# Kernel optimization log

Measured on AMD Instinct MI355X. Metric: run time of the kernel, lower is better.

The kernel has to match this reference:

```python
import jax, jax.numpy as jnp
import numpy as np

N = 50000       # nodes
E = 500000      # edges (before self-loops)
F_IN = 128      # node feature dim
F_E = 16        # edge feature dim
H = 8           # heads (conv1, conv2)
C1 = 32         # 256 // 8
C2 = 16         # 128 // 8
OUT = 1         # conv3 output channels (1 head, concat=False)
NS = 0.2        # leaky_relu negative slope
EPS = 1e-5      # batchnorm eps


def setup_inputs() -> dict:
    key = jax.random.key(0)
    ks = jax.random.split(key, 32)
    r = lambda k, s: jax.random.normal(k, s, jnp.float32) * 0.1
    inp = {
        'x': jax.random.normal(ks[0], (N, F_IN), jnp.float32),
        'edge_index': jax.random.randint(ks[1], (2, E), 0, N, jnp.int32),
        'edge_attr': jax.random.normal(ks[2], (E, F_E), jnp.float32),
        # conv1 (share_weights=True -> single lin)
        'W1': r(ks[3], (F_IN, H * C1)), 'b1': jnp.zeros((H * C1,), jnp.float32),
        'We1': r(ks[4], (F_E, H * C1)), 'att1': r(ks[5], (H, C1)),
        'bo1': jnp.zeros((H * C1,), jnp.float32),
        'g1': jnp.ones((H * C1,), jnp.float32), 'bt1': jnp.zeros((H * C1,), jnp.float32),
        # conv2 (share_weights=True)
        'W2': r(ks[6], (H * C1, H * C2)), 'b2': jnp.zeros((H * C2,), jnp.float32),
        'We2': r(ks[7], (F_E, H * C2)), 'att2': r(ks[8], (H, C2)),
        'bo2': jnp.zeros((H * C2,), jnp.float32),
        'g2': jnp.ones((H * C2,), jnp.float32), 'bt2': jnp.zeros((H * C2,), jnp.float32),
        # conv3 (share_weights=False -> separate lin_l / lin_r; 1 head, concat=False)
        'W3l': r(ks[9], (H * C2, OUT)), 'b3l': jnp.zeros((OUT,), jnp.float32),
        'W3r': r(ks[10], (H * C2, OUT)), 'b3r': jnp.zeros((OUT,), jnp.float32),
        'We3': r(ks[11], (F_E, OUT)), 'att3': r(ks[12], (1, OUT)),
        'bo3': jnp.zeros((OUT,), jnp.float32),
    }
    return inp


def _gatv2(x, src, dst, eattr, Wl, bl, Wr, br, We, att, bo, heads, ch, concat):
    """One GATv2Conv layer (PyG semantics), edges already include self-loops."""
    n = x.shape[0]
    xl = (x @ Wl + bl).reshape(n, heads, ch)              # source transform
    xr = (x @ Wr + br).reshape(n, heads, ch)              # target transform
    e = (eattr @ We).reshape(-1, heads, ch)               # edge transform (no bias)
    m = xl[src] + xr[dst] + e                             # [Etot, H, C]
    logit = jnp.einsum('ehc,hc->eh', jax.nn.leaky_relu(m, NS), att)
    lmax = jax.ops.segment_max(logit, dst, num_segments=n)
    ex = jnp.exp(logit - lmax[dst])
    denom = jax.ops.segment_sum(ex, dst, num_segments=n)
    alpha = ex / (denom[dst] + 1e-16)                     # segment softmax over dst
    out = jax.ops.segment_sum(alpha[:, :, None] * xl[src], dst, num_segments=n)
    out = out.reshape(n, heads * ch) if concat else out.mean(axis=1)
    return out + bo


def _bn(x, g, b):
    mu = x.mean(axis=0)
    var = ((x - mu) ** 2).mean(axis=0)
    return g * (x - mu) * jax.lax.rsqrt(var + EPS) + b


def reference(x, edge_index, edge_attr, W1, b1, We1, att1, bo1, g1, bt1,
              W2, b2, We2, att2, bo2, g2, bt2,
              W3l, b3l, W3r, b3r, We3, att3, bo3):
    n = x.shape[0]
    # add_self_loops=True with fill_value='mean' for edge_attr (PyG default)
    loop = jnp.arange(n, dtype=edge_index.dtype)
    src = jnp.concatenate([edge_index[0], loop])
    dst = jnp.concatenate([edge_index[1], loop])
    ea = jnp.concatenate([edge_attr,
                          jnp.broadcast_to(edge_attr.mean(axis=0), (n, edge_attr.shape[1]))], axis=0)

    h = _gatv2(x, src, dst, ea, W1, b1, W1, b1, We1, att1, bo1, H, C1, True)
    h = jax.nn.elu(_bn(h, g1, bt1))
    h = _gatv2(h, src, dst, ea, W2, b2, W2, b2, We2, att2, bo2, H, C2, True)
    h = jax.nn.elu(_bn(h, g2, bt2))
    out = _gatv2(h, src, dst, ea, W3l, b3l, W3r, b3r, We3, att3, bo3, 1, OUT, False)
    return out  # [N, 1]
```

## Files before the change

kernel.cpp:

```cpp
#include <hip/hip_runtime.h>

typedef unsigned short u16;
typedef __attribute__((ext_vector_type(4))) float f32x4;
typedef __attribute__((ext_vector_type(2))) float f32x2;
typedef __attribute__((ext_vector_type(8))) short bf16x8;

constexpr int Nn  = 50000;
constexpr int Ee  = 500000;
constexpr int ET  = Nn + Ee;
constexpr int FIN = 128;
constexpr int FE  = 16;
constexpr int Hh  = 8;
constexpr int C1  = 32, HC1 = 256;
constexpr int C2  = 16, HC2 = 128;
constexpr float NS  = 0.2f;
constexpr float EPS = 1e-5f;

__device__ __forceinline__ float b2f(u16 u) { return __uint_as_float(((unsigned)u) << 16); }
__device__ __forceinline__ u16 f2b(float f) {
  unsigned u = __float_as_uint(f);
  u += 0x7FFF + ((u >> 16) & 1);
  return (u16)(u >> 16);
}
__device__ __forceinline__ f32x2 ldbf2(const u16* p) {
  ushort2 u = *reinterpret_cast<const ushort2*>(p);
  return (f32x2){b2f(u.x), b2f(u.y)};
}
__device__ __forceinline__ void stbf2(u16* p, f32x2 v) {
  ushort2 u; u.x = f2b(v.x); u.y = f2b(v.y);
  *reinterpret_cast<ushort2*>(p) = u;
}

template <int RED>
__device__ __forceinline__ float red_sum(float v) {
  v += __int_as_float(__builtin_amdgcn_update_dpp(0, __float_as_int(v), 0xB1, 0xF, 0xF, true));
  v += __int_as_float(__builtin_amdgcn_update_dpp(0, __float_as_int(v), 0x4E, 0xF, 0xF, true));
  v += __int_as_float(__builtin_amdgcn_update_dpp(0, __float_as_int(v), 0x141, 0xF, 0xF, true));
  if constexpr (RED == 16)
    v += __int_as_float(__builtin_amdgcn_update_dpp(0, __float_as_int(v), 0x140, 0xF, 0xF, true));
  return v;
}

__global__ void k_init(int* __restrict__ deg, int* __restrict__ cursor, float* __restrict__ ea_mean,
                       float* __restrict__ bn1s, float* __restrict__ bn1q,
                       float* __restrict__ bn2s, float* __restrict__ bn2q) {
  int t = blockIdx.x * 256 + threadIdx.x;
  int stride = gridDim.x * 256;
  for (int i = t; i < Nn; i += stride) { deg[i] = 0; cursor[i] = 0; }
  if (t < FE) ea_mean[t] = 0.f;
  if (t >= 64 && t < 64 + HC1) { bn1s[t - 64] = 0.f; bn1q[t - 64] = 0.f; }
  if (t >= 384 && t < 384 + HC2) { bn2s[t - 384] = 0.f; bn2q[t - 384] = 0.f; }
}

__global__ void k_deg_mean(const int* __restrict__ ei, const float* __restrict__ ea,
                           int* __restrict__ deg, float* __restrict__ ea_mean) {
  int t = threadIdx.x;
  int e = blockIdx.x * 256 + t;
  if (e < ET) {
    int d = (e < Ee) ? ei[Ee + e] : (e - Ee);
    if ((unsigned)d >= (unsigned)Nn) d = 0;
    atomicAdd(&deg[d], 1);
  }
  __shared__ float s[256];
  int f  = t & 15;
  int r0 = (t >> 4) + blockIdx.x * 16;
  float acc = 0.f;
  for (int r = r0; r < Ee; r += gridDim.x * 16) acc += ea[r * FE + f];
  s[t] = acc;
  __syncthreads();
  if (t < 16) {
    float v = 0.f;
    for (int r = 0; r < 16; r++) v += s[r * 16 + t];
    atomicAdd(&ea_mean[t], v * (1.f / Ee));
  }
}

__global__ __launch_bounds__(1024) void k_scan(const int* __restrict__ deg, int* __restrict__ rowptr) {
  const int T = 1024;
  int t = threadIdx.x;
  const int CH = (Nn + T - 1) / T;
  int base = t * CH;
  int sum = 0;
  for (int i = 0; i < CH; i++) {
    int idx = base + i;
    if (idx < Nn) sum += deg[idx];
  }
  __shared__ int s[T];
  s[t] = sum;
  __syncthreads();
  for (int off = 1; off < T; off <<= 1) {
    int v = (t >= off) ? s[t - off] : 0;
    __syncthreads();
    s[t] += v;
    __syncthreads();
  }
  int run = (t == 0) ? 0 : s[t - 1];
  for (int i = 0; i < CH; i++) {
    int idx = base + i;
    if (idx < Nn) { rowptr[idx] = run; run += deg[idx]; }
  }
  if (t == T - 1) rowptr[Nn] = run;
}

__global__ void k_scatter(const int* __restrict__ ei, const int* __restrict__ rowptr,
                          int* __restrict__ cursor, int2* __restrict__ epack) {
  int e = blockIdx.x * 256 + threadIdx.x;
  if (e >= ET) return;
  int s, d;
  if (e < Ee) { s = ei[e]; d = ei[Ee + e]; } else { s = d = e - Ee; }
  if ((unsigned)s >= (unsigned)Nn) s = 0;
  if ((unsigned)d >= (unsigned)Nn) d = 0;
  int pos = rowptr[d] + atomicAdd(&cursor[d], 1);
  epack[pos] = make_int2(s, e);
}

__global__ void k_bn_coef(const float* __restrict__ sum, const float* __restrict__ sq,
                          const float* __restrict__ g, const float* __restrict__ bt,
                          float2* __restrict__ coef, int HC) {
  int ch = threadIdx.x;
  if (ch >= HC) return;
  float mu = sum[ch] * (1.f / Nn);
  float var = sq[ch] * (1.f / Nn) - mu * mu;
  float rs = rsqrtf(var + EPS);
  float sc = g[ch] * rs;
  coef[ch] = make_float2(sc, bt[ch] - sc * mu);
}

template <int HC>
__global__ void k_bn_stats(const u16* __restrict__ x, float* __restrict__ sum, float* __restrict__ sq) {
  long e0 = (long)blockIdx.x * 256 + threadIdx.x;
  long stride = (long)gridDim.x * 256;
  float s = 0.f, s2 = 0.f;
  for (long e = e0; e < (long)Nn * HC; e += stride) {
    float v = b2f(x[e]);
    s += v; s2 += v * v;
  }
  int ch = (int)(e0 % HC);
  atomicAdd(&sum[ch], s);
  atomicAdd(&sq[ch], s2);
}

template <int KK, int NN, typename AT, bool FUSE>
__global__ __launch_bounds__(256) void k_gemm_mfma(const AT* __restrict__ A, const float* __restrict__ W,
                                                   const float* __restrict__ bias, u16* __restrict__ C,
                                                   const float2* __restrict__ coef, int M) {
  constexpr int WT = KK + 8;
  __shared__ u16 Wt[64 * WT];
  int tid = threadIdx.x;
  int col0 = blockIdx.x * 64;
  int row0 = blockIdx.y * 64;
  for (int idx = tid; idx < KK * 64; idx += 256) {
    int k = idx >> 6, c = idx & 63;
    Wt[c * WT + k] = f2b(W[(size_t)k * NN + col0 + c]);
  }
  __syncthreads();
  int lane = tid & 63;
  int w = tid >> 6;
  int mr = lane & 15, quad = lane >> 4;
  int row = row0 + w * 16 + mr;
  f32x4 acc[4];
#pragma unroll
  for (int t = 0; t < 4; t++) acc[t] = (f32x4){0.f, 0.f, 0.f, 0.f};
  union Frag { bf16x8 v; u16 u[8]; };
  for (int kb = 0; kb < KK; kb += 32) {
    Frag a;
    if (row < M) {
      if constexpr (sizeof(AT) == 4) {
        const float* ap = (const float*)&A[(size_t)row * KK + kb + quad * 8];
        float4 a0 = *reinterpret_cast<const float4*>(ap);
        float4 a1 = *reinterpret_cast<const float4*>(ap + 4);
        a.u[0] = f2b(a0.x); a.u[1] = f2b(a0.y); a.u[2] = f2b(a0.z); a.u[3] = f2b(a0.w);
        a.u[4] = f2b(a1.x); a.u[5] = f2b(a1.y); a.u[6] = f2b(a1.z); a.u[7] = f2b(a1.w);
      } else {
        a.v = *reinterpret_cast<const bf16x8*>(&A[(size_t)row * KK + kb + quad * 8]);
        if constexpr (FUSE) {
          int k0 = kb + quad * 8;
#pragma unroll
          for (int j = 0; j < 8; j++) {
            float2 c2 = coef[k0 + j];
            float y = b2f(a.u[j]) * c2.x + c2.y;
            y = y > 0.f ? y : __expf(y) - 1.f;
            a.u[j] = f2b(y);
          }
        }
      }
    } else {
#pragma unroll
      for (int j = 0; j < 8; j++) a.u[j] = 0;
    }
#pragma unroll
    for (int t = 0; t < 4; t++) {
      const bf16x8* bp = reinterpret_cast<const bf16x8*>(&Wt[(t * 16 + mr) * WT + kb + quad * 8]);
      acc[t] = __builtin_amdgcn_mfma_f32_16x16x32_bf16(a.v, *bp, acc[t], 0, 0, 0);
    }
  }
  int orow = row0 + w * 16 + quad * 4;
#pragma unroll
  for (int t = 0; t < 4; t++) {
    int col = col0 + t * 16 + mr;
    float bs = bias[col];
#pragma unroll
    for (int r = 0; r < 4; r++) {
      int rr = orow + r;
      if (rr < M) C[(size_t)rr * NN + col] = f2b(acc[t][r] + bs);
    }
  }
}

template <int HC, int C, int WPN>
__global__ __launch_bounds__(256) void k_node_attn(
    const int* __restrict__ rowptr, const int2* __restrict__ epack,
    const u16* __restrict__ xl, const float* __restrict__ We, const float* __restrict__ att,
    const float* __restrict__ edge_attr, const float* __restrict__ ea_mean,
    const float* __restrict__ bo, u16* __restrict__ out) {
  int lane = threadIdx.x & 63;
  int gwid = (blockIdx.x << 2) + (threadIdx.x >> 6);
  int nwaves = gridDim.x << 2;
  int w = gwid % WPN;
  int i0 = gwid / WPN;
  int istride = nwaves / WPN;
  int c0 = w * 128 + lane * 2;
  f32x2 w2[FE];
#pragma unroll
  for (int k = 0; k < FE; k++) {
    float2 t = *reinterpret_cast<const float2*>(&We[k * HC + c0]);
    w2[k] = (f32x2){t.x, t.y};
  }
  float at0 = att[c0], at1 = att[c0 + 1];
  f32x2 ews2 = {0.f, 0.f};
#pragma unroll
  for (int k = 0; k < FE; k++) ews2 += ea_mean[k] * w2[k];
  float b0 = bo[c0], b1 = bo[c0 + 1];
  constexpr int RED = C / 2;
  constexpr int UN = 4;

  auto edge_ew = [&](int eid) -> f32x2 {
    if (eid < Ee) {
      const float4* ep = reinterpret_cast<const float4*>(&edge_attr[(size_t)eid * FE]);
      f32x2 a = {0.f, 0.f};
#pragma unroll
      for (int k4 = 0; k4 < 4; k4++) {
        float4 u = ep[k4];
        a += u.x * w2[4 * k4 + 0];
        a += u.y * w2[4 * k4 + 1];
        a += u.z * w2[4 * k4 + 2];
        a += u.w * w2[4 * k4 + 3];
      }
      return a;
    }
    return ews2;
  };

  if (i0 >= Nn) return;
  int p0 = rowptr[i0], p1 = rowptr[i0 + 1];
  ushort2 xdr = *reinterpret_cast<const ushort2*>(&xl[(size_t)i0 * HC + c0]);

  for (int i = i0; i < Nn;) {
    int inext = i + istride;
    int np0 = 0, np1 = 0;
    ushort2 nxdr = make_ushort2(0, 0);
    if (inext < Nn) {
      np0 = rowptr[inext];
      np1 = rowptr[inext + 1];
      nxdr = *reinterpret_cast<const ushort2*>(&xl[(size_t)inext * HC + c0]);
    }
    f32x2 xd = (f32x2){b2f(xdr.x), b2f(xdr.y)};
    int nb = (p1 - p0 + UN - 1) >> 2;
    float m = -1e30f, l = 0.f;
    f32x2 acc = {0.f, 0.f};

    int2 se[UN];
    int pb = p0;
#pragma unroll
    for (int j = 0; j < UN; j++) se[j] = epack[min(pb + j, p1 - 1)];

    for (int b = 0; b < nb; b++) {
      int sA[UN], eA[UN];
#pragma unroll
      for (int j = 0; j < UN; j++) {
        sA[j] = __builtin_amdgcn_readfirstlane(se[j].x);
        eA[j] = __builtin_amdgcn_readfirstlane(se[j].y);
      }
      ushort2 xr[UN];
#pragma unroll
      for (int j = 0; j < UN; j++)
        xr[j] = *reinterpret_cast<const ushort2*>(&xl[(size_t)sA[j] * HC + c0]);
      int pn = pb + UN;
      if (pn < p1) {
#pragma unroll
        for (int j = 0; j < UN; j++) se[j] = epack[min(pn + j, p1 - 1)];
      }
      f32x2 ew[UN];
#pragma unroll
      for (int j = 0; j < UN; j++) ew[j] = edge_ew(eA[j]);
      f32x2 xs[UN];
      float part[UN];
#pragma unroll
      for (int j = 0; j < UN; j++) {
        xs[j] = (f32x2){b2f(xr[j].x), b2f(xr[j].y)};
        f32x2 t = xs[j] + xd + ew[j];
        f32x2 tn = t * NS;
        f32x2 lk = {fmaxf(t.x, tn.x), fmaxf(t.y, tn.y)};
        float pt = lk.x * at0 + lk.y * at1;
        pt = red_sum<RED>(pt);
        part[j] = (pb + j < p1) ? pt : -1e30f;
      }
      float mn = m;
#pragma unroll
      for (int j = 0; j < UN; j++) mn = fmaxf(mn, part[j]);
      float sc = __expf(m - mn);
      float a[UN], asum = 0.f;
      f32x2 ax = {0.f, 0.f};
#pragma unroll
      for (int j = 0; j < UN; j++) {
        a[j] = __expf(part[j] - mn);
        asum += a[j];
        ax += a[j] * xs[j];
      }
      l = l * sc + asum;
      acc = acc * sc + ax;
      m = mn;
      pb = pn;
    }
    float inv = 1.f / (l + 1e-16f);
    f32x2 v = {acc.x * inv + b0, acc.y * inv + b1};
    stbf2(&out[(size_t)i * HC + c0], v);
    i = inext; p0 = np0; p1 = np1; xdr = nxdr;
  }
}

__global__ __launch_bounds__(256) void k_gemv3(const u16* __restrict__ h2,
                                               const float2* __restrict__ coef,
                                               const float* __restrict__ W3l, const float* __restrict__ b3l,
                                               const float* __restrict__ W3r, const float* __restrict__ b3r,
                                               float* __restrict__ xl3, float* __restrict__ xr3) {
  int lane = threadIdx.x & 63;
  int i = (blockIdx.x << 2) + (threadIdx.x >> 6);
  if (i >= Nn) return;
  float2 ca = coef[lane], cb = coef[64 + lane];
  float a = b2f(h2[(long)i * HC2 + lane]) * ca.x + ca.y;
  a = a > 0.f ? a : __expf(a) - 1.f;
  float b = b2f(h2[(long)i * HC2 + 64 + lane]) * cb.x + cb.y;
  b = b > 0.f ? b : __expf(b) - 1.f;
  float pl = a * W3l[lane] + b * W3l[64 + lane];
  float pr = a * W3r[lane] + b * W3r[64 + lane];
  for (int o = 1; o < 64; o <<= 1) { pl += __shfl_xor(pl, o); pr += __shfl_xor(pr, o); }
  if (lane == 0) { xl3[i] = pl + b3l[0]; xr3[i] = pr + b3r[0]; }
}

__global__ __launch_bounds__(256) void k_final3(
    const int* __restrict__ rowptr, const int2* __restrict__ epack,
    const float* __restrict__ xl3, const float* __restrict__ xr3,
    const float* __restrict__ We3, const float* __restrict__ att3,
    const float* __restrict__ edge_attr, const float* __restrict__ ea_mean,
    const float* __restrict__ bo3, float* __restrict__ out) {
  int lane = threadIdx.x & 63;
  int i = (blockIdx.x << 2) + (threadIdx.x >> 6);
  if (i >= Nn) return;
  float we[FE];
#pragma unroll
  for (int k4 = 0; k4 < 4; k4++) {
    float4 u = reinterpret_cast<const float4*>(We3)[k4];
    we[4 * k4] = u.x; we[4 * k4 + 1] = u.y; we[4 * k4 + 2] = u.z; we[4 * k4 + 3] = u.w;
  }
  float at = att3[0];
  float ews = 0.f;
#pragma unroll
  for (int k = 0; k < FE; k++) ews += ea_mean[k] * we[k];
  float xd = xr3[i];
  int p0 = rowptr[i], p1 = rowptr[i + 1];
  float m = -1e30f, l = 0.f, o = 0.f;
  for (int p = p0 + lane; p < p1; p += 64) {
    int2 se = epack[p];
    int s = se.x, eid = se.y;
    float ew;
    if (eid < Ee) {
      const float4* ep = reinterpret_cast<const float4*>(&edge_attr[(size_t)eid * FE]);
      ew = 0.f;
#pragma unroll
      for (int k4 = 0; k4 < 4; k4++) {
        float4 u = ep[k4];
        ew += u.x * we[4 * k4] + u.y * we[4 * k4 + 1] + u.z * we[4 * k4 + 2] + u.w * we[4 * k4 + 3];
      }
    } else ew = ews;
    float xsv = xl3[s];
    float t = xsv + xd + ew;
    float v = t > 0.f ? t : NS * t;
    float logit = v * at;
    float mn = fmaxf(m, logit);
    float sc = __expf(m - mn);
    float a = __expf(logit - mn);
    l = l * sc + a;
    o = o * sc + a * xsv;
    m = mn;
  }
  float M = m;
#pragma unroll
  for (int off = 1; off < 64; off <<= 1) M = fmaxf(M, __shfl_xor(M, off));
  float adj = __expf(m - M);
  float lw = l * adj, ow = o * adj;
#pragma unroll
  for (int off = 1; off < 64; off <<= 1) { lw += __shfl_xor(lw, off); ow += __shfl_xor(ow, off); }
  if (lane == 0) out[i] = ow / (lw + 1e-16f) + bo3[0];
}

extern "C" void kernel_launch(void* const* d_in, const int* in_sizes, int n_in,
                              void* d_out, int out_size, void* d_ws, size_t ws_size,
                              hipStream_t stream) {
  const float* x    = (const float*)d_in[0];
  const int*   ei   = (const int*)d_in[1];
  const float* ea   = (const float*)d_in[2];
  const float* W1   = (const float*)d_in[3];
  const float* b1   = (const float*)d_in[4];
  const float* We1  = (const float*)d_in[5];
  const float* att1 = (const float*)d_in[6];
  const float* bo1  = (const float*)d_in[7];
  const float* g1   = (const float*)d_in[8];
  const float* bt1  = (const float*)d_in[9];
  const float* W2   = (const float*)d_in[10];
  const float* b2   = (const float*)d_in[11];
  const float* We2  = (const float*)d_in[12];
  const float* att2 = (const float*)d_in[13];
  const float* bo2  = (const float*)d_in[14];
  const float* g2   = (const float*)d_in[15];
  const float* bt2  = (const float*)d_in[16];
  const float* W3l  = (const float*)d_in[17];
  const float* b3l  = (const float*)d_in[18];
  const float* W3r  = (const float*)d_in[19];
  const float* b3r  = (const float*)d_in[20];
  const float* We3  = (const float*)d_in[21];
  const float* att3 = (const float*)d_in[22];
  const float* bo3  = (const float*)d_in[23];
  float* out = (float*)d_out;

  char* ws = (char*)d_ws;
  size_t off = 0;
  auto alloc = [&](size_t bytes) -> void* {
    void* p = ws + off;
    off = (off + bytes + 255) & ~(size_t)255;
    return p;
  };
  int*    deg     = (int*)alloc((size_t)Nn * 4);
  int*    rowptr  = (int*)alloc((size_t)(Nn + 1) * 4);
  int*    cursor  = (int*)alloc((size_t)Nn * 4);
  int2*   epack   = (int2*)alloc((size_t)ET * 8);
  float*  ea_mean = (float*)alloc((size_t)FE * 4);
  float*  bn1s    = (float*)alloc(256 * 4);
  float*  bn1q    = (float*)alloc(256 * 4);
  float*  bn2s    = (float*)alloc(128 * 4);
  float*  bn2q    = (float*)alloc(128 * 4);
  float2* bncoef  = (float2*)alloc(256 * 8);
  float*  xl3     = (float*)alloc((size_t)Nn * 4);
  float*  xr3     = (float*)alloc((size_t)Nn * 4);
  u16*    xlA     = (u16*)alloc((size_t)Nn * 256 * 2);
  u16*    hB      = (u16*)alloc((size_t)Nn * 256 * 2);

  k_init<<<512, 256, 0, stream>>>(deg, cursor, ea_mean, bn1s, bn1q, bn2s, bn2q);
  k_deg_mean<<<(ET + 255) / 256, 256, 0, stream>>>(ei, ea, deg, ea_mean);
  k_scan<<<1, 1024, 0, stream>>>(deg, rowptr);
  k_scatter<<<(ET + 255) / 256, 256, 0, stream>>>(ei, rowptr, cursor, epack);

  k_gemm_mfma<FIN, HC1, float, false><<<dim3(HC1 / 64, (Nn + 63) / 64), 256, 0, stream>>>(
      x, W1, b1, xlA, nullptr, Nn);
  k_node_attn<HC1, C1, 2><<<2048, 256, 0, stream>>>(rowptr, epack, xlA, We1, att1,
                                                    ea, ea_mean, bo1, hB);
  k_bn_stats<HC1><<<256, 256, 0, stream>>>(hB, bn1s, bn1q);
  k_bn_coef<<<1, 256, 0, stream>>>(bn1s, bn1q, g1, bt1, bncoef, HC1);

  k_gemm_mfma<HC1, HC2, u16, true><<<dim3(HC2 / 64, (Nn + 63) / 64), 256, 0, stream>>>(
      hB, W2, b2, xlA, bncoef, Nn);
  k_node_attn<HC2, C2, 1><<<2048, 256, 0, stream>>>(rowptr, epack, xlA, We2, att2,
                                                    ea, ea_mean, bo2, hB);
  k_bn_stats<HC2><<<256, 256, 0, stream>>>(hB, bn2s, bn2q);
  k_bn_coef<<<1, 256, 0, stream>>>(bn2s, bn2q, g2, bt2, bncoef, HC2);

  k_gemv3<<<(Nn + 3) / 4, 256, 0, stream>>>(hB, bncoef, W3l, b3l, W3r, b3r, xl3, xr3);
  k_final3<<<(Nn + 3) / 4, 256, 0, stream>>>(rowptr, epack, xl3, xr3, We3, att3,
                                             ea, ea_mean, bo3, out);
}
```

Before: 729.0 us.

## Stage edge attributes via async LDS loads, use exp2, shrink final3 groups

The node attention kernel now double-buffers each edge block's 16-float edge attributes into shared memory with global_load_lds, prefetching the next block while the current one is computed. It also pads epack so the min() clamps can be dropped, and folds log2(e) into the attention weights so exp2 can replace expf. k_bn_stats reads two bf16 values per thread. k_final3 gives each node 16 lanes instead of 64 to cut idle lanes on low-degree nodes. The cost is added complexity from the manual vmcnt waits and the padded epack tail.

```diff
diff --git a/kernel.cpp b/kernel.cpp
--- a/kernel.cpp
+++ b/kernel.cpp
@@ -15,16 +15,13 @@
 constexpr int C2  = 16, HC2 = 128;
 constexpr float NS  = 0.2f;
 constexpr float EPS = 1e-5f;
+constexpr float LOG2E = 1.44269504088896340736f;
 
 __device__ __forceinline__ float b2f(u16 u) { return __uint_as_float(((unsigned)u) << 16); }
 __device__ __forceinline__ u16 f2b(float f) {
   unsigned u = __float_as_uint(f);
   u += 0x7FFF + ((u >> 16) & 1);
   return (u16)(u >> 16);
-}
-__device__ __forceinline__ f32x2 ldbf2(const u16* p) {
-  ushort2 u = *reinterpret_cast<const ushort2*>(p);
-  return (f32x2){b2f(u.x), b2f(u.y)};
 }
 __device__ __forceinline__ void stbf2(u16* p, f32x2 v) {
   ushort2 u; u.x = f2b(v.x); u.y = f2b(v.y);
@@ -106,6 +103,7 @@
                           int* __restrict__ cursor, int2* __restrict__ epack) {
   int e = blockIdx.x * 256 + threadIdx.x;
   if (e >= ET) return;
+  if (e < 4) epack[ET + e] = make_int2(0, Ee);
   int s, d;
   if (e < Ee) { s = ei[e]; d = ei[Ee + e]; } else { s = d = e - Ee; }
   if ((unsigned)s >= (unsigned)Nn) s = 0;
@@ -128,16 +126,17 @@
 
 template <int HC>
 __global__ void k_bn_stats(const u16* __restrict__ x, float* __restrict__ sum, float* __restrict__ sq) {
-  long e0 = (long)blockIdx.x * 256 + threadIdx.x;
-  long stride = (long)gridDim.x * 256;
-  float s = 0.f, s2 = 0.f;
-  for (long e = e0; e < (long)Nn * HC; e += stride) {
-    float v = b2f(x[e]);
-    s += v; s2 += v * v;
-  }
-  int ch = (int)(e0 % HC);
-  atomicAdd(&sum[ch], s);
-  atomicAdd(&sq[ch], s2);
+  long i0 = ((long)blockIdx.x * 256 + threadIdx.x) * 2;
+  long stride = (long)gridDim.x * 512;
+  float s0 = 0.f, q0 = 0.f, s1 = 0.f, q1 = 0.f;
+  for (long e = i0; e < (long)Nn * HC; e += stride) {
+    ushort2 u = *reinterpret_cast<const ushort2*>(&x[e]);
+    float v0 = b2f(u.x), v1 = b2f(u.y);
+    s0 += v0; q0 += v0 * v0; s1 += v1; q1 += v1 * v1;
+  }
+  int ch = (int)(i0 % HC);
+  atomicAdd(&sum[ch], s0); atomicAdd(&sq[ch], q0);
+  atomicAdd(&sum[ch + 1], s1); atomicAdd(&sq[ch + 1], q1);
 }
 
 template <int KK, int NN, typename AT, bool FUSE>
@@ -213,8 +212,10 @@
     const u16* __restrict__ xl, const float* __restrict__ We, const float* __restrict__ att,
     const float* __restrict__ edge_attr, const float* __restrict__ ea_mean,
     const float* __restrict__ bo, u16* __restrict__ out) {
+  __shared__ float sea[4][2][4][16];
   int lane = threadIdx.x & 63;
-  int gwid = (blockIdx.x << 2) + (threadIdx.x >> 6);
+  int widx = threadIdx.x >> 6;
+  int gwid = (blockIdx.x << 2) + widx;
   int nwaves = gridDim.x << 2;
   int w = gwid % WPN;
   int i0 = gwid / WPN;
@@ -226,7 +227,7 @@
     float2 t = *reinterpret_cast<const float2*>(&We[k * HC + c0]);
     w2[k] = (f32x2){t.x, t.y};
   }
-  float at0 = att[c0], at1 = att[c0 + 1];
+  float at0 = att[c0] * LOG2E, at1 = att[c0 + 1] * LOG2E;
   f32x2 ews2 = {0.f, 0.f};
 #pragma unroll
   for (int k = 0; k < FE; k++) ews2 += ea_mean[k] * w2[k];
@@ -234,9 +235,22 @@
   constexpr int RED = C / 2;
   constexpr int UN = 4;
 
-  auto edge_ew = [&](int eid) -> f32x2 {
+  auto stage = [&](const int2* sep, int buf) {
+    int y01 = (lane & 4) ? sep[1].y : sep[0].y;
+    int y23 = (lane & 4) ? sep[3].y : sep[2].y;
+    int eidv = (lane & 8) ? y23 : y01;
+    int ec = (eidv < Ee) ? eidv : 0;
+    const float* src = edge_attr + (size_t)ec * FE + (lane & 3) * 4;
+    if (lane < 16) {
+      __builtin_amdgcn_global_load_lds(
+          (const __attribute__((address_space(1))) unsigned int*)src,
+          (__attribute__((address_space(3))) unsigned int*)&sea[widx][buf][0][0],
+          16, 0, 0);
+    }
+  };
+  auto ea_dot_lds = [&](int eid, int buf, int jj) -> f32x2 {
     if (eid < Ee) {
-      const float4* ep = reinterpret_cast<const float4*>(&edge_attr[(size_t)eid * FE]);
+      const float4* ep = reinterpret_cast<const float4*>(&sea[widx][buf][jj][0]);
       f32x2 a = {0.f, 0.f};
 #pragma unroll
       for (int k4 = 0; k4 < 4; k4++) {
@@ -270,11 +284,14 @@
     f32x2 acc = {0.f, 0.f};
 
     int2 se[UN];
+#pragma unroll
+    for (int j = 0; j < UN; j++) se[j] = epack[p0 + j];
+    stage(se, 0);
+
     int pb = p0;
-#pragma unroll
-    for (int j = 0; j < UN; j++) se[j] = epack[min(pb + j, p1 - 1)];
-
     for (int b = 0; b < nb; b++) {
+      int buf = b & 1;
+      asm volatile("s_waitcnt vmcnt(0)" ::: "memory");
       int sA[UN], eA[UN];
 #pragma unroll
       for (int j = 0; j < UN; j++) {
@@ -286,34 +303,34 @@
       for (int j = 0; j < UN; j++)
         xr[j] = *reinterpret_cast<const ushort2*>(&xl[(size_t)sA[j] * HC + c0]);
       int pn = pb + UN;
-      if (pn < p1) {
-#pragma unroll
-        for (int j = 0; j < UN; j++) se[j] = epack[min(pn + j, p1 - 1)];
-      }
-      f32x2 ew[UN];
-#pragma unroll
-      for (int j = 0; j < UN; j++) ew[j] = edge_ew(eA[j]);
+      bool more = pn < p1;
+      if (more) {
+#pragma unroll
+        for (int j = 0; j < UN; j++) se[j] = epack[pn + j];
+      }
       f32x2 xs[UN];
       float part[UN];
 #pragma unroll
       for (int j = 0; j < UN; j++) {
+        f32x2 ew = ea_dot_lds(eA[j], buf, j);
         xs[j] = (f32x2){b2f(xr[j].x), b2f(xr[j].y)};
-        f32x2 t = xs[j] + xd + ew[j];
+        f32x2 t = xs[j] + xd + ew;
         f32x2 tn = t * NS;
         f32x2 lk = {fmaxf(t.x, tn.x), fmaxf(t.y, tn.y)};
         float pt = lk.x * at0 + lk.y * at1;
         pt = red_sum<RED>(pt);
         part[j] = (pb + j < p1) ? pt : -1e30f;
       }
+      if (more) stage(se, buf ^ 1);
       float mn = m;
 #pragma unroll
       for (int j = 0; j < UN; j++) mn = fmaxf(mn, part[j]);
-      float sc = __expf(m - mn);
+      float sc = __builtin_amdgcn_exp2f(m - mn);
       float a[UN], asum = 0.f;
       f32x2 ax = {0.f, 0.f};
 #pragma unroll
       for (int j = 0; j < UN; j++) {
-        a[j] = __expf(part[j] - mn);
+        a[j] = __builtin_amdgcn_exp2f(part[j] - mn);
         asum += a[j];
         ax += a[j] * xs[j];
       }
@@ -354,8 +371,9 @@
     const float* __restrict__ We3, const float* __restrict__ att3,
     const float* __restrict__ edge_attr, const float* __restrict__ ea_mean,
     const float* __restrict__ bo3, float* __restrict__ out) {
-  int lane = threadIdx.x & 63;
-  int i = (blockIdx.x << 2) + (threadIdx.x >> 6);
+  int t = threadIdx.x;
+  int lane16 = t & 15;
+  int i = blockIdx.x * 16 + (t >> 4);
   if (i >= Nn) return;
   float we[FE];
 #pragma unroll
@@ -370,7 +388,7 @@
   float xd = xr3[i];
   int p0 = rowptr[i], p1 = rowptr[i + 1];
   float m = -1e30f, l = 0.f, o = 0.f;
-  for (int p = p0 + lane; p < p1; p += 64) {
+  for (int p = p0 + lane16; p < p1; p += 16) {
     int2 se = epack[p];
     int s = se.x, eid = se.y;
     float ew;
@@ -384,8 +402,8 @@
       }
     } else ew = ews;
     float xsv = xl3[s];
-    float t = xsv + xd + ew;
-    float v = t > 0.f ? t : NS * t;
+    float tt = xsv + xd + ew;
+    float v = tt > 0.f ? tt : NS * tt;
     float logit = v * at;
     float mn = fmaxf(m, logit);
     float sc = __expf(m - mn);
@@ -396,12 +414,12 @@
   }
   float M = m;
 #pragma unroll
-  for (int off = 1; off < 64; off <<= 1) M = fmaxf(M, __shfl_xor(M, off));
+  for (int off = 1; off < 16; off <<= 1) M = fmaxf(M, __shfl_xor(M, off));
   float adj = __expf(m - M);
   float lw = l * adj, ow = o * adj;
 #pragma unroll
-  for (int off = 1; off < 64; off <<= 1) { lw += __shfl_xor(lw, off); ow += __shfl_xor(ow, off); }
-  if (lane == 0) out[i] = ow / (lw + 1e-16f) + bo3[0];
+  for (int off = 1; off < 16; off <<= 1) { lw += __shfl_xor(lw, off); ow += __shfl_xor(ow, off); }
+  if (lane16 == 0) out[i] = ow / (lw + 1e-16f) + bo3[0];
 }
 
 extern "C" void kernel_launch(void* const* d_in, const int* in_sizes, int n_in,
@@ -443,7 +461,7 @@
   int*    deg     = (int*)alloc((size_t)Nn * 4);
   int*    rowptr  = (int*)alloc((size_t)(Nn + 1) * 4);
   int*    cursor  = (int*)alloc((size_t)Nn * 4);
-  int2*   epack   = (int2*)alloc((size_t)ET * 8);
+  int2*   epack   = (int2*)alloc((size_t)(ET + 4) * 8);
   float*  ea_mean = (float*)alloc((size_t)FE * 4);
   float*  bn1s    = (float*)alloc(256 * 4);
   float*  bn1q    = (float*)alloc(256 * 4);
@@ -475,6 +493,6 @@
   k_bn_coef<<<1, 256, 0, stream>>>(bn2s, bn2q, g2, bt2, bncoef, HC2);
 
   k_gemv3<<<(Nn + 3) / 4, 256, 0, stream>>>(hB, bncoef, W3l, b3l, W3r, b3r, xl3, xr3);
-  k_final3<<<(Nn + 3) / 4, 256, 0, stream>>>(rowptr, epack, xl3, xr3, We3, att3,
-                                             ea, ea_mean, bo3, out);
-}
+  k_final3<<<(Nn + 15) / 16, 256, 0, stream>>>(rowptr, epack, xl3, xr3, We3, att3,
+                                               ea, ea_mean, bo3, out);
+}
```

Measured after the change: 728.1 us. Within noise of the previous version (-0.1%).
